# Kernel tuning notes

Hardware: AMD Instinct MI355X
Metric: run time of the kernel (lower is better)

Reference implementation:

```python
import jax, jax.numpy as jnp
import numpy as np

E = 4096      # hidden_size
H = 32        # num_attention_heads
D = E // H    # head_dim = 128
PAST = 8191   # past kv length


def setup_inputs() -> dict:
    key = jax.random.key(0)
    ks = jax.random.split(key, 10)
    s = 0.02
    return {
        "hidden_states": jax.random.normal(ks[0], (1, 1, E), jnp.float32),
        "past_key": jax.random.normal(ks[1], (1, D, PAST), jnp.float32),
        "past_value": jax.random.normal(ks[2], (1, PAST, D), jnp.float32),
        "attention_mask": jnp.zeros((1, 1, 1, PAST + 1), jnp.float32),
        "q_w": jax.random.normal(ks[3], (E, E), jnp.float32) * s,
        "q_b": jnp.zeros((E,), jnp.float32),
        "kv_w": jax.random.normal(ks[4], (E, 2 * D), jnp.float32) * s,
        "kv_b": jnp.zeros((2 * D,), jnp.float32),
        "proj_w": jax.random.normal(ks[5], (E, E), jnp.float32) * s,
        "proj_b": jnp.zeros((E,), jnp.float32),
    }


def reference(hidden_states, past_key, past_value, attention_mask,
              q_w, q_b, kv_w, kv_b, proj_w, proj_b):
    B, S = hidden_states.shape[:2]  # B=1, S=1 (decode)
    # Conv1D projections: x @ W + b
    query = hidden_states @ q_w + q_b            # [B, S, E]
    kv = hidden_states @ kv_w + kv_b             # [B, S, 2D]
    key_new, value_new = kv[..., :D], kv[..., D:]  # [B, S, D] each

    q = query.reshape(B, S, H, D).transpose(0, 2, 1, 3)  # [B, H, S, D]
    key_perm = key_new.transpose(0, 2, 1)                 # [B, D, S]
    full_key = jnp.concatenate([past_key, key_perm], axis=-1)     # [B, D, K]
    full_value = jnp.concatenate([past_value, value_new], axis=-2)  # [B, K, D]
    K = full_key.shape[-1]

    # QK^T with shared single KV head, scaled by sqrt(head_dim)
    scores = jnp.einsum('bhqd,bdk->bhqk', q, full_key)  # [B, H, S, K]
    scores = scores / jnp.asarray(D ** 0.5, scores.dtype)

    # causal mask over rows [K-S, K)
    causal = (jnp.arange(K)[None, :] <= (jnp.arange(S) + (K - S))[:, None])  # [S, K]
    mask_value = jnp.asarray(jnp.finfo(scores.dtype).min, scores.dtype)
    scores = jnp.where(causal[None, None], scores, mask_value)
    scores = scores + attention_mask

    attn_weights = jax.nn.softmax(scores, axis=-1)                # [B, H, S, K]
    attn_out = jnp.einsum('bhqk,bkd->bhqd', attn_weights, full_value)  # [B, H, S, D]
    attn_out = attn_out.transpose(0, 2, 1, 3).reshape(B, S, E)    # merge heads
    attn_out = attn_out @ proj_w + proj_b                          # [B, S, E]
    return attn_out, key_perm, value_new
```

## Files before the change

### kernel.cpp

```cpp
#include <hip/hip_runtime.h>
#include <math.h>

#define E_DIM 4096
#define H_NUM 32
#define D_DIM 128
#define PAST_K 8191
#define K_TOT 8192

#define WS_QUERY  0
#define WS_KV     4096
#define WS_E      8192
#define WS_L      (WS_E + H_NUM * K_TOT)
#define WS_ATTN   (WS_L + 64)

__global__ void k_init(float* __restrict__ ws, float* __restrict__ out) {
    int i = blockIdx.x * 256 + threadIdx.x;
    if (i < E_DIM) {
        ws[WS_QUERY + i] = 0.f;
        ws[WS_ATTN + i]  = 0.f;
        out[i] = 0.f;
    }
    if (i < 256) ws[WS_KV + i] = 0.f;
    if (i < 32)  ws[WS_L + i] = 0.f;
}

__global__ void k_qkv(const float* __restrict__ hs,
                      const float* __restrict__ q_w, const float* __restrict__ q_b,
                      const float* __restrict__ kv_w, const float* __restrict__ kv_b,
                      float* __restrict__ ws) {
    const int t = threadIdx.x;
    const int e0 = blockIdx.y * 32;
    if (blockIdx.x < 4) {
        const int o = blockIdx.x * 1024 + t * 4;
        float ax = 0.f, ay = 0.f, az = 0.f, aw = 0.f;
#pragma unroll
        for (int i = 0; i < 32; ++i) {
            const int e = e0 + i;
            const float x = hs[e];
            const float4 w = *reinterpret_cast<const float4*>(q_w + (size_t)e * E_DIM + o);
            ax += x * w.x; ay += x * w.y; az += x * w.z; aw += x * w.w;
        }
        if (blockIdx.y == 0) {
            const float4 b = *reinterpret_cast<const float4*>(q_b + o);
            ax += b.x; ay += b.y; az += b.z; aw += b.w;
        }
        float* y = ws + WS_QUERY + o;
        atomicAdd(y + 0, ax); atomicAdd(y + 1, ay);
        atomicAdd(y + 2, az); atomicAdd(y + 3, aw);
    } else {
        if (t >= 64) return;
        const int o = t * 4;
        float ax = 0.f, ay = 0.f, az = 0.f, aw = 0.f;
#pragma unroll
        for (int i = 0; i < 32; ++i) {
            const int e = e0 + i;
            const float x = hs[e];
            const float4 w = *reinterpret_cast<const float4*>(kv_w + (size_t)e * 256 + o);
            ax += x * w.x; ay += x * w.y; az += x * w.z; aw += x * w.w;
        }
        if (blockIdx.y == 0) {
            const float4 b = *reinterpret_cast<const float4*>(kv_b + o);
            ax += b.x; ay += b.y; az += b.z; aw += b.w;
        }
        float* y = ws + WS_KV + o;
        atomicAdd(y + 0, ax); atomicAdd(y + 1, ay);
        atomicAdd(y + 2, az); atomicAdd(y + 3, aw);
    }
}

__global__ void k_scores(const float* __restrict__ past_key,
                         const float* __restrict__ mask,
                         float* __restrict__ ws,
                         float* __restrict__ out) {
    __shared__ float part[4 * 8 * 256];
    const int t = threadIdx.x;
    const int lane = t & 63;
    const int team = t >> 6;
    const int d0 = __builtin_amdgcn_readfirstlane(team * 32);
    const int h0 = blockIdx.y * 8;
    const int k0 = blockIdx.x * 256;
    const int kq = k0 + lane * 4;
    const float* __restrict__ qb  = ws + WS_QUERY + h0 * D_DIM;
    const float* __restrict__ kvn = ws + WS_KV;

    float4 acc[8];
#pragma unroll
    for (int h = 0; h < 8; ++h) acc[h] = make_float4(0.f, 0.f, 0.f, 0.f);

    const bool tail = (kq + 3 >= PAST_K);
#pragma unroll 8
    for (int i = 0; i < 32; ++i) {
        const int d = d0 + i;
        const float* kp = past_key + (size_t)d * PAST_K + kq;
        const float* p3 = tail ? (kvn + d) : (kp + 3);
        const float va = kp[0], vb = kp[1], vc = kp[2], vd = *p3;
#pragma unroll
        for (int h = 0; h < 8; ++h) {
            const float qv = qb[h * D_DIM + d];
            acc[h].x += qv * va; acc[h].y += qv * vb;
            acc[h].z += qv * vc; acc[h].w += qv * vd;
        }
    }
#pragma unroll
    for (int h = 0; h < 8; ++h)
        *reinterpret_cast<float4*>(&part[((team * 8 + h) * 64 + lane) * 4]) = acc[h];
    __syncthreads();

    if (t < 64) {
        const float scale = 0.08838834764831845f;
        const float4 mk = *reinterpret_cast<const float4*>(mask + kq);
#pragma unroll
        for (int h = 0; h < 8; ++h) {
            float4 s = *reinterpret_cast<float4*>(&part[((0 * 8 + h) * 64 + lane) * 4]);
#pragma unroll
            for (int tm = 1; tm < 4; ++tm) {
                const float4 r = *reinterpret_cast<float4*>(&part[((tm * 8 + h) * 64 + lane) * 4]);
                s.x += r.x; s.y += r.y; s.z += r.z; s.w += r.w;
            }
            float4 e;
            e.x = __expf(s.x * scale + mk.x);
            e.y = __expf(s.y * scale + mk.y);
            e.z = __expf(s.z * scale + mk.z);
            e.w = __expf(s.w * scale + mk.w);
            *reinterpret_cast<float4*>(ws + WS_E + (size_t)(h0 + h) * K_TOT + kq) = e;
            float lsum = e.x + e.y + e.z + e.w;
#pragma unroll
            for (int off = 32; off > 0; off >>= 1) lsum += __shfl_xor(lsum, off);
            if (lane == 0) atomicAdd(ws + WS_L + h0 + h, lsum);
        }
    }
    if (blockIdx.x == 0 && blockIdx.y == 0) out[E_DIM + t] = kvn[t];
}

__global__ void k_pv(const float* __restrict__ past_value, float* __restrict__ ws) {
    __shared__ float smem[8192];
    const int t = threadIdx.x;
    const int h0 = blockIdx.y * 8;
    const int k0 = blockIdx.x * 256;

#pragma unroll
    for (int i = 0; i < 8; ++i) {
        const float rl = 1.0f / ws[WS_L + h0 + i];
        smem[i * 256 + t] = ws[WS_E + (size_t)(h0 + i) * K_TOT + k0 + t] * rl;
    }
    __syncthreads();

    const int g  = t >> 5;
    const int dq = t & 31;
    const int d4 = dq * 4;
    const float* __restrict__ vnew = ws + WS_KV + D_DIM;

    float4 acc[8];
#pragma unroll
    for (int h = 0; h < 8; ++h) acc[h] = make_float4(0.f, 0.f, 0.f, 0.f);

#pragma unroll 8
    for (int kl = 0; kl < 32; ++kl) {
        const int k = k0 + g * 32 + kl;
        const float* vp = (k < PAST_K) ? (past_value + (size_t)k * D_DIM + d4)
                                       : (vnew + d4);
        const float4 v = *reinterpret_cast<const float4*>(vp);
#pragma unroll
        for (int h = 0; h < 8; ++h) {
            const float p = smem[h * 256 + g * 32 + kl];
            acc[h].x += p * v.x; acc[h].y += p * v.y;
            acc[h].z += p * v.z; acc[h].w += p * v.w;
        }
    }
    __syncthreads();
#pragma unroll
    for (int h = 0; h < 8; ++h)
        *reinterpret_cast<float4*>(&smem[((g * 8 + h) * 32 + dq) * 4]) = acc[h];
    __syncthreads();

    const int hh = t >> 5;
    float4 s = make_float4(0.f, 0.f, 0.f, 0.f);
#pragma unroll
    for (int gg = 0; gg < 8; ++gg) {
        const float4 r = *reinterpret_cast<float4*>(&smem[((gg * 8 + hh) * 32 + dq) * 4]);
        s.x += r.x; s.y += r.y; s.z += r.z; s.w += r.w;
    }
    float* a = ws + WS_ATTN + (h0 + hh) * D_DIM + d4;
    atomicAdd(a + 0, s.x); atomicAdd(a + 1, s.y);
    atomicAdd(a + 2, s.z); atomicAdd(a + 3, s.w);
}

__global__ void k_proj(const float* __restrict__ proj_w, const float* __restrict__ proj_b,
                       const float* __restrict__ ws, float* __restrict__ out) {
    const int t = threadIdx.x;
    const int o = blockIdx.x * 1024 + t * 4;
    const int e0 = blockIdx.y * 32;
    float ax = 0.f, ay = 0.f, az = 0.f, aw = 0.f;
#pragma unroll
    for (int i = 0; i < 32; ++i) {
        const int e = e0 + i;
        const float x = ws[WS_ATTN + e];
        const float4 w = *reinterpret_cast<const float4*>(proj_w + (size_t)e * E_DIM + o);
        ax += x * w.x; ay += x * w.y; az += x * w.z; aw += x * w.w;
    }
    if (blockIdx.y == 0) {
        const float4 b = *reinterpret_cast<const float4*>(proj_b + o);
        ax += b.x; ay += b.y; az += b.z; aw += b.w;
    }
    atomicAdd(out + o + 0, ax); atomicAdd(out + o + 1, ay);
    atomicAdd(out + o + 2, az); atomicAdd(out + o + 3, aw);
}

extern "C" void kernel_launch(void* const* d_in, const int* in_sizes, int n_in,
                              void* d_out, int out_size, void* d_ws, size_t ws_size,
                              hipStream_t stream) {
    const float* hs      = (const float*)d_in[0];
    const float* past_k  = (const float*)d_in[1];
    const float* past_v  = (const float*)d_in[2];
    const float* mask    = (const float*)d_in[3];
    const float* q_w     = (const float*)d_in[4];
    const float* q_b     = (const float*)d_in[5];
    const float* kv_w    = (const float*)d_in[6];
    const float* kv_b    = (const float*)d_in[7];
    const float* proj_w  = (const float*)d_in[8];
    const float* proj_b  = (const float*)d_in[9];
    float* out = (float*)d_out;
    float* ws  = (float*)d_ws;

    k_init  <<<dim3(16),     dim3(256), 0, stream>>>(ws, out);
    k_qkv   <<<dim3(5, 128), dim3(256), 0, stream>>>(hs, q_w, q_b, kv_w, kv_b, ws);
    k_scores<<<dim3(32, 4),  dim3(256), 0, stream>>>(past_k, mask, ws, out);
    k_pv    <<<dim3(32, 4),  dim3(256), 0, stream>>>(past_v, ws);
    k_proj  <<<dim3(4, 128), dim3(256), 0, stream>>>(proj_w, proj_b, ws, out);
}
```

Baseline: 227.2 us.

## Fuse scores and PV into one attention kernel, defer softmax normalization to projection

Merges the score/exp kernel and the probability-times-value kernel into a single kernel. Each block computes exp scores for a 128-key tile, keeps them in shared memory, and immediately accumulates them against V. This removes the 1 MB global round-trip of exp scores and one launch. Because the global row sum is not known inside the fused kernel, normalization moves into k_proj, which divides by the per-head sum. The trade-off is that each block now does more sequential work across two phases, and the grid doubles to 256 blocks.

```diff
diff --git a/kernel.cpp b/kernel.cpp
--- a/kernel.cpp
+++ b/kernel.cpp
@@ -7,21 +7,16 @@
 #define PAST_K 8191
 #define K_TOT 8192
 
-#define WS_QUERY  0
-#define WS_KV     4096
-#define WS_E      8192
-#define WS_L      (WS_E + H_NUM * K_TOT)
-#define WS_ATTN   (WS_L + 64)
+#define WS_QUERY 0
+#define WS_KV    4096
+#define WS_L     4352
+#define WS_ATTN  4416
+#define WS_ZEND  8512
 
 __global__ void k_init(float* __restrict__ ws, float* __restrict__ out) {
     int i = blockIdx.x * 256 + threadIdx.x;
-    if (i < E_DIM) {
-        ws[WS_QUERY + i] = 0.f;
-        ws[WS_ATTN + i]  = 0.f;
-        out[i] = 0.f;
-    }
-    if (i < 256) ws[WS_KV + i] = 0.f;
-    if (i < 32)  ws[WS_L + i] = 0.f;
+    if (i < WS_ZEND) ws[i] = 0.f;
+    if (i < E_DIM) out[i] = 0.f;
 }
 
 __global__ void k_qkv(const float* __restrict__ hs,
@@ -68,121 +63,110 @@
     }
 }
 
-__global__ void k_scores(const float* __restrict__ past_key,
-                         const float* __restrict__ mask,
-                         float* __restrict__ ws,
-                         float* __restrict__ out) {
-    __shared__ float part[4 * 8 * 256];
-    const int t = threadIdx.x;
-    const int lane = t & 63;
-    const int team = t >> 6;
-    const int d0 = __builtin_amdgcn_readfirstlane(team * 32);
-    const int h0 = blockIdx.y * 8;
-    const int k0 = blockIdx.x * 256;
-    const int kq = k0 + lane * 4;
-    const float* __restrict__ qb  = ws + WS_QUERY + h0 * D_DIM;
-    const float* __restrict__ kvn = ws + WS_KV;
-
-    float4 acc[8];
-#pragma unroll
-    for (int h = 0; h < 8; ++h) acc[h] = make_float4(0.f, 0.f, 0.f, 0.f);
-
-    const bool tail = (kq + 3 >= PAST_K);
-#pragma unroll 8
-    for (int i = 0; i < 32; ++i) {
-        const int d = d0 + i;
-        const float* kp = past_key + (size_t)d * PAST_K + kq;
-        const float* p3 = tail ? (kvn + d) : (kp + 3);
-        const float va = kp[0], vb = kp[1], vc = kp[2], vd = *p3;
-#pragma unroll
-        for (int h = 0; h < 8; ++h) {
-            const float qv = qb[h * D_DIM + d];
-            acc[h].x += qv * va; acc[h].y += qv * vb;
-            acc[h].z += qv * vc; acc[h].w += qv * vd;
-        }
-    }
-#pragma unroll
-    for (int h = 0; h < 8; ++h)
-        *reinterpret_cast<float4*>(&part[((team * 8 + h) * 64 + lane) * 4]) = acc[h];
-    __syncthreads();
-
-    if (t < 64) {
-        const float scale = 0.08838834764831845f;
-        const float4 mk = *reinterpret_cast<const float4*>(mask + kq);
-#pragma unroll
-        for (int h = 0; h < 8; ++h) {
-            float4 s = *reinterpret_cast<float4*>(&part[((0 * 8 + h) * 64 + lane) * 4]);
-#pragma unroll
-            for (int tm = 1; tm < 4; ++tm) {
-                const float4 r = *reinterpret_cast<float4*>(&part[((tm * 8 + h) * 64 + lane) * 4]);
-                s.x += r.x; s.y += r.y; s.z += r.z; s.w += r.w;
-            }
-            float4 e;
-            e.x = __expf(s.x * scale + mk.x);
-            e.y = __expf(s.y * scale + mk.y);
-            e.z = __expf(s.z * scale + mk.z);
-            e.w = __expf(s.w * scale + mk.w);
-            *reinterpret_cast<float4*>(ws + WS_E + (size_t)(h0 + h) * K_TOT + kq) = e;
-            float lsum = e.x + e.y + e.z + e.w;
-#pragma unroll
-            for (int off = 32; off > 0; off >>= 1) lsum += __shfl_xor(lsum, off);
-            if (lane == 0) atomicAdd(ws + WS_L + h0 + h, lsum);
-        }
-    }
-    if (blockIdx.x == 0 && blockIdx.y == 0) out[E_DIM + t] = kvn[t];
-}
-
-__global__ void k_pv(const float* __restrict__ past_value, float* __restrict__ ws) {
-    __shared__ float smem[8192];
+__global__ void k_attn(const float* __restrict__ past_key,
+                       const float* __restrict__ past_value,
+                       const float* __restrict__ mask,
+                       float* __restrict__ ws,
+                       float* __restrict__ out) {
+    __shared__ float sq[8 * 128];
+    __shared__ float sp[8 * 128];
+    __shared__ float red[8 * 8 * 32 * 4];
     const int t = threadIdx.x;
     const int h0 = blockIdx.y * 8;
-    const int k0 = blockIdx.x * 256;
-
-#pragma unroll
-    for (int i = 0; i < 8; ++i) {
-        const float rl = 1.0f / ws[WS_L + h0 + i];
-        smem[i * 256 + t] = ws[WS_E + (size_t)(h0 + i) * K_TOT + k0 + t] * rl;
-    }
-    __syncthreads();
-
-    const int g  = t >> 5;
+    const int k0 = blockIdx.x * 128;
+    const float* __restrict__ kvn = ws + WS_KV;
+
+#pragma unroll
+    for (int i = 0; i < 4; ++i) sq[i * 256 + t] = ws[WS_QUERY + h0 * D_DIM + i * 256 + t];
+    __syncthreads();
+
+    const int team = __builtin_amdgcn_readfirstlane((t >> 7) & 1);
+    const int kl = t & 127;
+    const int k = k0 + kl;
+    const int d0 = team * 64;
+    const bool tailA = (k == PAST_K);
+    const float* kp = tailA ? (kvn + d0) : (past_key + (size_t)d0 * PAST_K + k);
+    const size_t kstride = tailA ? 1 : PAST_K;
+
+    float acc[8];
+#pragma unroll
+    for (int h = 0; h < 8; ++h) acc[h] = 0.f;
+
+#pragma unroll 4
+    for (int i = 0; i < 64; i += 4) {
+        const float kv0 = kp[0];
+        const float kv1 = kp[kstride];
+        const float kv2 = kp[2 * kstride];
+        const float kv3 = kp[3 * kstride];
+        kp += 4 * kstride;
+#pragma unroll
+        for (int h = 0; h < 8; ++h) {
+            const float4 qv = *reinterpret_cast<const float4*>(&sq[h * 128 + d0 + i]);
+            acc[h] += qv.x * kv0 + qv.y * kv1 + qv.z * kv2 + qv.w * kv3;
+        }
+    }
+
+    float* part = red;
+    if (team == 1) {
+#pragma unroll
+        for (int h = 0; h < 8; ++h) part[h * 128 + kl] = acc[h];
+    }
+    __syncthreads();
+    if (team == 0) {
+        const float scale = 0.08838834764831845f;
+        const float mk = mask[k];
+#pragma unroll
+        for (int h = 0; h < 8; ++h) {
+            const float s = acc[h] + part[h * 128 + kl];
+            const float e = __expf(s * scale + mk);
+            sp[h * 128 + kl] = e;
+            float lsum = e;
+#pragma unroll
+            for (int off = 32; off > 0; off >>= 1) lsum += __shfl_xor(lsum, off);
+            if ((t & 63) == 0) atomicAdd(ws + WS_L + h0 + h, lsum);
+        }
+    }
+    __syncthreads();
+
+    const int kg = t >> 5;
     const int dq = t & 31;
     const int d4 = dq * 4;
-    const float* __restrict__ vnew = ws + WS_KV + D_DIM;
-
-    float4 acc[8];
-#pragma unroll
-    for (int h = 0; h < 8; ++h) acc[h] = make_float4(0.f, 0.f, 0.f, 0.f);
-
-#pragma unroll 8
-    for (int kl = 0; kl < 32; ++kl) {
-        const int k = k0 + g * 32 + kl;
-        const float* vp = (k < PAST_K) ? (past_value + (size_t)k * D_DIM + d4)
-                                       : (vnew + d4);
+    const float* __restrict__ vnew = kvn + D_DIM;
+
+    float4 vacc[8];
+#pragma unroll
+    for (int h = 0; h < 8; ++h) vacc[h] = make_float4(0.f, 0.f, 0.f, 0.f);
+
+#pragma unroll 4
+    for (int kk = 0; kk < 16; ++kk) {
+        const int k2 = k0 + kg * 16 + kk;
+        const float* vp = (k2 < PAST_K) ? (past_value + (size_t)k2 * D_DIM + d4)
+                                        : (vnew + d4);
         const float4 v = *reinterpret_cast<const float4*>(vp);
 #pragma unroll
         for (int h = 0; h < 8; ++h) {
-            const float p = smem[h * 256 + g * 32 + kl];
-            acc[h].x += p * v.x; acc[h].y += p * v.y;
-            acc[h].z += p * v.z; acc[h].w += p * v.w;
-        }
-    }
-    __syncthreads();
+            const float p = sp[h * 128 + kg * 16 + kk];
+            vacc[h].x += p * v.x; vacc[h].y += p * v.y;
+            vacc[h].z += p * v.z; vacc[h].w += p * v.w;
+        }
+    }
 #pragma unroll
     for (int h = 0; h < 8; ++h)
-        *reinterpret_cast<float4*>(&smem[((g * 8 + h) * 32 + dq) * 4]) = acc[h];
+        *reinterpret_cast<float4*>(&red[((kg * 8 + h) * 32 + dq) * 4]) = vacc[h];
     __syncthreads();
 
     const int hh = t >> 5;
     float4 s = make_float4(0.f, 0.f, 0.f, 0.f);
 #pragma unroll
     for (int gg = 0; gg < 8; ++gg) {
-        const float4 r = *reinterpret_cast<float4*>(&smem[((gg * 8 + hh) * 32 + dq) * 4]);
+        const float4 r = *reinterpret_cast<const float4*>(&red[((gg * 8 + hh) * 32 + dq) * 4]);
         s.x += r.x; s.y += r.y; s.z += r.z; s.w += r.w;
     }
     float* a = ws + WS_ATTN + (h0 + hh) * D_DIM + d4;
     atomicAdd(a + 0, s.x); atomicAdd(a + 1, s.y);
     atomicAdd(a + 2, s.z); atomicAdd(a + 3, s.w);
+
+    if (blockIdx.x == 0 && blockIdx.y == 0) out[E_DIM + t] = kvn[t];
 }
 
 __global__ void k_proj(const float* __restrict__ proj_w, const float* __restrict__ proj_b,
@@ -194,7 +178,7 @@
 #pragma unroll
     for (int i = 0; i < 32; ++i) {
         const int e = e0 + i;
-        const float x = ws[WS_ATTN + e];
+        const float x = ws[WS_ATTN + e] / ws[WS_L + (e >> 7)];
         const float4 w = *reinterpret_cast<const float4*>(proj_w + (size_t)e * E_DIM + o);
         ax += x * w.x; ay += x * w.y; az += x * w.z; aw += x * w.w;
     }
@@ -222,9 +206,8 @@
     float* out = (float*)d_out;
     float* ws  = (float*)d_ws;
 
-    k_init  <<<dim3(16),     dim3(256), 0, stream>>>(ws, out);
-    k_qkv   <<<dim3(5, 128), dim3(256), 0, stream>>>(hs, q_w, q_b, kv_w, kv_b, ws);
-    k_scores<<<dim3(32, 4),  dim3(256), 0, stream>>>(past_k, mask, ws, out);
-    k_pv    <<<dim3(32, 4),  dim3(256), 0, stream>>>(past_v, ws);
-    k_proj  <<<dim3(4, 128), dim3(256), 0, stream>>>(proj_w, proj_b, ws, out);
-}
+    k_init<<<dim3(34),     dim3(256), 0, stream>>>(ws, out);
+    k_qkv <<<dim3(5, 128), dim3(256), 0, stream>>>(hs, q_w, q_b, kv_w, kv_b, ws);
+    k_attn<<<dim3(64, 4),  dim3(256), 0, stream>>>(past_k, past_v, mask, ws, out);
+    k_proj<<<dim3(4, 128), dim3(256), 0, stream>>>(proj_w, proj_b, ws, out);
+}
```

Measured after the change: 238.1 us. 1.05x slower.
